# Kernel optimization log

Hardware: AMD Instinct MI355X
Metric: run time of the kernel (lower is better)

Reference implementation:

```python
import jax
import jax.numpy as jnp
from jax import lax
import numpy as np

EMBED_DIM = 768
NUM_HEADS = 12
BATCH = 8
SEQ = 1024
EPS = 1e-07
QK_QBIT = 8
QK_KBIT = 8
AV_ABIT = 8
AV_VBIT = 8
PROJ_WBIT = 8
PROJ_XBIT = 8
SCALE = EMBED_DIM ** (-0.5)  # module uses embed_dim, not head_dim


def _ste(hard, soft):
    # straight-through estimator: forward = hard, backward grad = d(soft)
    return soft + lax.stop_gradient(hard - soft)


def fake_quant_signed(x, bit):
    # _quantize_signed_matrix_train: sign/abs, global-max scaling, STE clamp + round
    sign = lax.stop_gradient(jnp.sign(x))
    a = jnp.abs(x)
    scaling = lax.stop_gradient(jnp.max(a)) + EPS
    y = a / scaling
    y = _ste(jnp.clip(y, 0.0, 1.0), y)          # Clamp.apply (STE)
    levels = 2.0 ** (bit - 1.0) - 1.0
    y = _ste(jnp.round(y * levels) / levels, y)  # Round.apply (STE)
    return y * scaling * sign


def fake_quant_unsigned(x, bit):
    # _quantize_unsigned_matrix_train
    scaling = lax.stop_gradient(jnp.max(x)) + EPS
    y = x / scaling
    y = _ste(jnp.clip(y, 0.0, 1.0), y)
    levels = 2.0 ** bit - 1.0
    y = _ste(jnp.round(y * levels) / levels, y)
    return y * scaling


def asim_linear(x, w, b, wbit, xbit):
    # ASiMLinear in 'Train' mode with signed_act=True: fake-quantize activation
    # and weight, dense matmul, trim_noise=0 -> no perturbation.
    xq = fake_quant_signed(x, xbit)
    wq = fake_quant_signed(w, wbit)
    return jnp.einsum('bnc,oc->bno', xq, wq) + b


def setup_inputs() -> dict:
    key = jax.random.key(0)
    k_x, k_qw, k_qb, k_pw, k_pb = jax.random.split(key, 5)
    x = jax.random.normal(k_x, (BATCH, SEQ, EMBED_DIM), dtype=jnp.float32)
    s = 1.0 / np.sqrt(EMBED_DIM)
    qkv_w = jax.random.normal(k_qw, (3 * EMBED_DIM, EMBED_DIM), dtype=jnp.float32) * s
    qkv_b = jax.random.normal(k_qb, (3 * EMBED_DIM,), dtype=jnp.float32) * 0.01
    proj_w = jax.random.normal(k_pw, (EMBED_DIM, EMBED_DIM), dtype=jnp.float32) * s
    proj_b = jax.random.normal(k_pb, (EMBED_DIM,), dtype=jnp.float32) * 0.01
    return {'x': x, 'qkv_w': qkv_w, 'qkv_b': qkv_b, 'proj_w': proj_w, 'proj_b': proj_b}


def reference(x, qkv_w, qkv_b, proj_w, proj_b):
    B, N, C = x.shape
    H = NUM_HEADS
    D = C // H
    # qkv projection (ASiMLinear, Train mode)
    qkv = asim_linear(x, qkv_w, qkv_b, PROJ_WBIT, PROJ_XBIT)      # [B, N, 3C]
    qkv = qkv.reshape(B, N, 3, H, D).transpose(2, 0, 3, 1, 4)      # [3, B, H, N, D]
    q, k, v = qkv[0], qkv[1], qkv[2]
    # _qk_train: fake-quantize q and k^T, matmul (trim_noise=0 -> no perturb)
    qq = fake_quant_signed(q, QK_QBIT)
    kq = fake_quant_signed(jnp.swapaxes(k, -2, -1), QK_KBIT)
    attn = jnp.einsum('bhnd,bhdm->bhnm', qq, kq) * SCALE           # [B, H, N, N]
    attn = jax.nn.softmax(attn, axis=-1)
    # dropout ratio 0.0 -> identity
    # _av_train: unsigned fake-quant of attention, signed fake-quant of v
    aq = fake_quant_unsigned(attn, AV_ABIT)
    vq = fake_quant_signed(v, AV_VBIT)
    out = jnp.einsum('bhnm,bhmd->bhnd', aq, vq)                    # [B, H, N, D]
    out = out.transpose(0, 2, 1, 3).reshape(B, N, C)
    # output projection (ASiMLinear, Train mode)
    out = asim_linear(out, proj_w, proj_b, PROJ_WBIT, PROJ_XBIT)
    return out
```

## Files before the change

kernel.cpp:

```cpp
#include <hip/hip_runtime.h>
#include <hip/hip_bf16.h>
#include <cstdint>
#include <cstddef>

#define B_    8
#define SEQ_  1024
#define C_    768
#define H_    12
#define D_    64
#define TC_   2304
#define M_    8192
#define EPS_  1e-7f
#define SCALE_ 0.036084391824351615f

typedef __attribute__((ext_vector_type(8))) short bf16x8;
typedef __attribute__((ext_vector_type(4))) float f32x4;

__device__ __forceinline__ bf16x8 expand8(int2 raw) {
  union { int2 v; signed char c[8]; } u; u.v = raw;
  bf16x8 r;
  #pragma unroll
  for (int j = 0; j < 8; ++j) {
    float f = (float)(int)u.c[j];
    r[j] = (short)(__float_as_uint(f) >> 16);
  }
  return r;
}
__device__ __forceinline__ void expand16(int4 raw, int4& lo, int4& hi) {
  union { int4 v; signed char c[16]; } u; u.v = raw;
  unsigned short s[16];
  #pragma unroll
  for (int j = 0; j < 16; ++j) {
    float f = (float)(int)u.c[j];
    s[j] = (unsigned short)(__float_as_uint(f) >> 16);
  }
  lo = *(const int4*)&s[0]; hi = *(const int4*)&s[8];
}

__global__ void k_init(float* g) {
  if (threadIdx.x == 0) {
    g[0]=0.f; g[1]=0.f; g[2]=0.f; g[3]=0.f; g[4]=0.f; g[5]=0.f;
    g[6]=3.402823466e+38f;
    g[7]=0.f;
  }
}

__global__ __launch_bounds__(256) void k_absmax_fused(const float4* __restrict__ x,
                                                      const float4* __restrict__ w1,
                                                      const float4* __restrict__ w2,
                                                      float* g) {
  __shared__ float red[4];
  const int blk = blockIdx.x;
  const float4* p; unsigned n4; float* gout; int b0, nb;
  if (blk < 384)      { p = x;  n4 = 1572864u; gout = &g[0]; b0 = 0;   nb = 384; }
  else if (blk < 480) { p = w1; n4 = 442368u;  gout = &g[1]; b0 = 384; nb = 96;  }
  else                { p = w2; n4 = 147456u;  gout = &g[2]; b0 = 480; nb = 48;  }
  float m = 0.f;
  for (unsigned i = (unsigned)(blk - b0) * 256u + threadIdx.x; i < n4; i += (unsigned)nb * 256u) {
    float4 v = p[i];
    m = fmaxf(m, fmaxf(fmaxf(fabsf(v.x), fabsf(v.y)), fmaxf(fabsf(v.z), fabsf(v.w))));
  }
  #pragma unroll
  for (int off = 32; off; off >>= 1) m = fmaxf(m, __shfl_xor(m, off));
  if ((threadIdx.x & 63) == 0) red[threadIdx.x >> 6] = m;
  __syncthreads();
  if (threadIdx.x == 0) {
    m = fmaxf(fmaxf(red[0], red[1]), fmaxf(red[2], red[3]));
    atomicMax((unsigned int*)gout, __float_as_uint(m));
  }
}

__device__ __forceinline__ void quant_seg8(const float* __restrict__ in, unsigned n, float s,
                                           int8_t* __restrict__ out, unsigned i0, unsigned stride) {
  for (unsigned i = i0; i < n; i += stride) {
    float v = in[i];
    float y = fminf(fabsf(v) / s, 1.0f);
    int q = (int)rintf(y * 127.0f);
    if (v < 0.f) q = -q;
    out[i] = (int8_t)q;
  }
}
__global__ __launch_bounds__(256) void k_quant_fused(const float* __restrict__ x,
                                                     const float* __restrict__ w1,
                                                     const float* __restrict__ w2,
                                                     const float* __restrict__ g,
                                                     int8_t* __restrict__ xq,
                                                     int8_t* __restrict__ wq,
                                                     int8_t* __restrict__ pw) {
  const int blk = blockIdx.x;
  if (blk < 1536)      quant_seg8(x,  6291456u, g[0] + EPS_, xq, (unsigned)blk * 256u + threadIdx.x, 1536u * 256u);
  else if (blk < 1968) quant_seg8(w1, 1769472u, g[1] + EPS_, wq, (unsigned)(blk - 1536) * 256u + threadIdx.x, 432u * 256u);
  else                 quant_seg8(w2,  589824u, g[2] + EPS_, pw, (unsigned)(blk - 1968) * 256u + threadIdx.x, 144u * 256u);
}

__global__ __launch_bounds__(256) void k_quant_i8(const float* __restrict__ in, unsigned n,
                                                  const float* __restrict__ gmax,
                                                  int8_t* __restrict__ out) {
  const float s = *gmax + EPS_;
  quant_seg8(in, n, s, out, blockIdx.x * blockDim.x + threadIdx.x, gridDim.x * blockDim.x);
}

__global__ __launch_bounds__(256) void k_gemm8(const int8_t* __restrict__ A,
                                               const int8_t* __restrict__ Bt,
                                               const float* __restrict__ bias,
                                               float* __restrict__ C,
                                               int Mn, int Nn, int Kn,
                                               const float* __restrict__ sA, const float* __restrict__ sB,
                                               float* pmax, int partDiv) {
  __shared__ unsigned short As[128 * 64];
  __shared__ unsigned short Bs[128 * 64];
  const int tid = threadIdx.x;
  int flat = blockIdx.y * gridDim.x + blockIdx.x;
  int chunk = (gridDim.x * gridDim.y) >> 3;
  int nf = (flat & 7) * chunk + (flat >> 3);
  const int n0 = (nf % gridDim.x) * 128, m0 = (nf / gridDim.x) * 128;
  const int wid = tid >> 6, lane = tid & 63;
  const int wr = wid >> 1, wc = wid & 1;
  const int lrow = lane & 15;
  const int lko = (lane >> 4) << 3;
  f32x4 acc[4][4] = {};
  const int r0 = tid >> 2;
  const int c0 = tid & 3;
  const int8_t* ga = A  + (size_t)m0 * Kn;
  const int8_t* gb = Bt + (size_t)n0 * Kn;
  const int nt = Kn >> 6;
  int4 ra0 = *(const int4*)(ga + (size_t)r0 * Kn + c0 * 16);
  int4 ra1 = *(const int4*)(ga + (size_t)(64 + r0) * Kn + c0 * 16);
  int4 rb0 = *(const int4*)(gb + (size_t)r0 * Kn + c0 * 16);
  int4 rb1 = *(const int4*)(gb + (size_t)(64 + r0) * Kn + c0 * 16);
  for (int t = 0; t < nt; ++t) {
    if (t) __syncthreads();
    {
      int4 lo, hi;
      const int sx0 = (r0 & 7) << 4;
      const int bb0 = r0 * 128 + c0 * 32;
      const int bb1 = (64 + r0) * 128 + c0 * 32;
      expand16(ra0, lo, hi);
      *(int4*)((char*)As + ( bb0       ^ sx0)) = lo;
      *(int4*)((char*)As + ((bb0 + 16) ^ sx0)) = hi;
      expand16(ra1, lo, hi);
      *(int4*)((char*)As + ( bb1       ^ sx0)) = lo;
      *(int4*)((char*)As + ((bb1 + 16) ^ sx0)) = hi;
      expand16(rb0, lo, hi);
      *(int4*)((char*)Bs + ( bb0       ^ sx0)) = lo;
      *(int4*)((char*)Bs + ((bb0 + 16) ^ sx0)) = hi;
      expand16(rb1, lo, hi);
      *(int4*)((char*)Bs + ( bb1       ^ sx0)) = lo;
      *(int4*)((char*)Bs + ((bb1 + 16) ^ sx0)) = hi;
    }
    if (t + 1 < nt) {
      const int ko = (t + 1) * 64;
      ra0 = *(const int4*)(ga + (size_t)r0 * Kn + ko + c0 * 16);
      ra1 = *(const int4*)(ga + (size_t)(64 + r0) * Kn + ko + c0 * 16);
      rb0 = *(const int4*)(gb + (size_t)r0 * Kn + ko + c0 * 16);
      rb1 = *(const int4*)(gb + (size_t)(64 + r0) * Kn + ko + c0 * 16);
    }
    __syncthreads();
    #pragma unroll
    for (int kk = 0; kk < 64; kk += 32) {
      bf16x8 af[4], bfr[4];
      #pragma unroll
      for (int i = 0; i < 4; ++i) {
        int row = wr * 64 + i * 16 + lrow;
        af[i] = *(const bf16x8*)((const char*)As + ((row * 128 + (kk + lko) * 2) ^ ((row & 7) << 4)));
      }
      #pragma unroll
      for (int j = 0; j < 4; ++j) {
        int row = wc * 64 + j * 16 + lrow;
        bfr[j] = *(const bf16x8*)((const char*)Bs + ((row * 128 + (kk + lko) * 2) ^ ((row & 7) << 4)));
      }
      #pragma unroll
      for (int i = 0; i < 4; ++i)
        #pragma unroll
        for (int j = 0; j < 4; ++j)
          acc[i][j] = __builtin_amdgcn_mfma_f32_16x16x32_bf16(af[i], bfr[j], acc[i][j], 0, 0, 0);
    }
  }
  const float alpha = (sA[0] + EPS_) * (sB[0] + EPS_) * (1.0f / 16129.0f);
  const int orow = (lane >> 4) << 2;
  float amax = 0.f;
  #pragma unroll
  for (int i = 0; i < 4; ++i) {
    #pragma unroll
    for (int j = 0; j < 4; ++j) {
      int col = n0 + wc * 64 + j * 16 + lrow;
      float bc = bias[col];
      #pragma unroll
      for (int rr = 0; rr < 4; ++rr) {
        int row = m0 + wr * 64 + i * 16 + orow + rr;
        float val = acc[i][j][rr] * alpha + bc;
        C[(size_t)row * Nn + col] = val;
        amax = fmaxf(amax, fabsf(val));
      }
    }
  }
  if (pmax) {
    #pragma unroll
    for (int off = 32; off; off >>= 1) amax = fmaxf(amax, __shfl_xor(amax, off));
    if (lane == 0) atomicMax((unsigned int*)&pmax[n0 / partDiv], __float_as_uint(amax));
  }
}

__global__ __launch_bounds__(256) void k_quant_heads(const float* __restrict__ qkvf, const float* __restrict__ g,
                                                     int8_t* __restrict__ qo, int8_t* __restrict__ ko,
                                                     int8_t* __restrict__ vT) {
  const unsigned total = (unsigned)M_ * TC_;
  const float s0 = g[3] + EPS_, s1 = g[4] + EPS_, s2 = g[5] + EPS_;
  for (unsigned i = blockIdx.x * blockDim.x + threadIdx.x; i < total; i += gridDim.x * blockDim.x) {
    unsigned m = i / 2304u, o = i % 2304u;
    unsigned part = o / 768u, c = o % 768u;
    unsigned h = c >> 6, d = c & 63;
    unsigned b = m >> 10, n = m & 1023;
    float s = (part == 0) ? s0 : (part == 1) ? s1 : s2;
    float v = qkvf[i];
    float y = fminf(fabsf(v) / s, 1.0f);
    int q = (int)rintf(y * 127.0f);
    if (v < 0.f) q = -q;
    unsigned bh = b * 12 + h;
    if (part == 0)      qo[((size_t)bh * 1024 + n) * 64 + d] = (int8_t)q;
    else if (part == 1) ko[((size_t)bh * 1024 + n) * 64 + d] = (int8_t)q;
    else                vT[((size_t)bh * 64 + d) * 1024 + n] = (int8_t)q;
  }
}

__global__ __launch_bounds__(256) void k_attn_stats_mfma(
    const int8_t* __restrict__ qi8, const int8_t* __restrict__ ki8,
    const float* __restrict__ g, float* __restrict__ rowmax, float* __restrict__ denomv,
    unsigned int* __restrict__ gminden) {
  __shared__ unsigned short Ks[64 * 64];
  __shared__ float red[4];
  const int bh = blockIdx.x >> 4, rt = blockIdx.x & 15;
  const int tid = threadIdx.x, w = tid >> 6, lane = tid & 63;
  const int lrow = lane & 15, lko = (lane >> 4) << 3;
  const int8_t* qbase = qi8 + (size_t)bh * 65536;
  const int8_t* kbase = ki8 + (size_t)bh * 65536;
  bf16x8 qf[2];
  #pragma unroll
  for (int ks = 0; ks < 2; ++ks)
    qf[ks] = expand8(*(const int2*)(qbase + (size_t)(rt*64 + w*16 + lrow) * 64 + ks*32 + lko));
  const float qkScale = (g[3] + EPS_) * (g[4] + EPS_) * (1.0f / 16129.0f) * SCALE_;
  float m = -3.0e38f, den = 0.f;
  const int srow = tid >> 2, sc = tid & 3;
  const int sx = (srow & 7) << 4;
  int4 kraw = *(const int4*)(kbase + (size_t)srow * 64 + sc * 16);
  for (int t = 0; t < 16; ++t) {
    __syncthreads();
    {
      int4 lo, hi; expand16(kraw, lo, hi);
      int bb = srow * 128 + sc * 32;
      *(int4*)((char*)Ks + ( bb       ^ sx)) = lo;
      *(int4*)((char*)Ks + ((bb + 16) ^ sx)) = hi;
    }
    if (t < 15)
      kraw = *(const int4*)(kbase + (size_t)(t + 1) * 4096 + (size_t)srow * 64 + sc * 16);
    __syncthreads();
    f32x4 acc[4] = {};
    #pragma unroll
    for (int ks = 0; ks < 2; ++ks)
      #pragma unroll
      for (int j = 0; j < 4; ++j) {
        int row = j * 16 + lrow;
        bf16x8 kf = *(const bf16x8*)((const char*)Ks + ((row * 128 + (ks*32 + lko) * 2) ^ ((row & 7) << 4)));
        acc[j] = __builtin_amdgcn_mfma_f32_16x16x32_bf16(kf, qf[ks], acc[j], 0, 0, 0);
      }
    float mnew = m;
    #pragma unroll
    for (int j = 0; j < 4; ++j)
      #pragma unroll
      for (int rr = 0; rr < 4; ++rr)
        mnew = fmaxf(mnew, acc[j][rr] * qkScale);
    float d = den * __expf(m - mnew);
    #pragma unroll
    for (int j = 0; j < 4; ++j)
      #pragma unroll
      for (int rr = 0; rr < 4; ++rr)
        d += __expf(acc[j][rr] * qkScale - mnew);
    den = d; m = mnew;
  }
  #pragma unroll
  for (int off = 16; off <= 32; off <<= 1) {
    float mo = __shfl_xor(m, off);
    float doo = __shfl_xor(den, off);
    float mg = fmaxf(m, mo);
    den = den * __expf(m - mg) + doo * __expf(mo - mg);
    m = mg;
  }
  if (lane < 16) {
    size_t rg = (size_t)bh * 1024 + rt * 64 + w * 16 + lane;
    rowmax[rg] = m;
    denomv[rg] = den;
  }
  float bm = den;
  #pragma unroll
  for (int off = 1; off < 16; off <<= 1) bm = fminf(bm, __shfl_xor(bm, off));
  if (lane == 0) red[w] = bm;
  __syncthreads();
  if (tid == 0)
    atomicMin(gminden, __float_as_uint(fminf(fminf(red[0], red[1]), fminf(red[2], red[3]))));
}

__global__ __launch_bounds__(256) void k_attn_pv_mfma(
    const int8_t* __restrict__ qi8, const int8_t* __restrict__ ki8, const int8_t* __restrict__ vti8,
    const float* __restrict__ g, const unsigned int* __restrict__ gminden,
    const float* __restrict__ rowmax, const float* __restrict__ denomv,
    float* __restrict__ aof, float* __restrict__ gamax) {
  __shared__ unsigned short Ks[64 * 64];
  __shared__ unsigned short Vs[64 * 64];
  __shared__ unsigned short Ps[64 * 64];
  __shared__ float red[4];
  const int bh = blockIdx.x >> 4, rt = blockIdx.x & 15;
  const int b = bh / 12, h = bh % 12;
  const int tid = threadIdx.x, w = tid >> 6, lane = tid & 63;
  const int lrow = lane & 15, lko = (lane >> 4) << 3;
  const int8_t* qbase = qi8 + (size_t)bh * 65536;
  const int8_t* kbase = ki8 + (size_t)bh * 65536;
  const int8_t* vbase = vti8 + (size_t)bh * 65536;
  bf16x8 qf[2];
  #pragma unroll
  for (int ks = 0; ks < 2; ++ks)
    qf[ks] = expand8(*(const int2*)(qbase + (size_t)(rt*64 + w*16 + lrow) * 64 + ks*32 + lko));
  const float qkScale = (g[3] + EPS_) * (g[4] + EPS_) * (1.0f / 16129.0f) * SCALE_;
  const float minden = __uint_as_float(*gminden);
  const float sa = 1.0f / minden + EPS_;
  const float invSa = 1.0f / sa;
  const float sv = g[5] + EPS_;
  const float pvScale = sa * sv * (1.0f / 32385.0f);
  const float rm  = rowmax[(size_t)bh * 1024 + rt * 64 + w * 16 + lrow];
  const float ivd = 1.0f / denomv[(size_t)bh * 1024 + rt * 64 + w * 16 + lrow];
  f32x4 accO[4] = {};
  const int srow = tid >> 2, sc = tid & 3;
  const int sx = (srow & 7) << 4;
  int4 kraw = *(const int4*)(kbase + (size_t)srow * 64 + sc * 16);
  int4 vraw = *(const int4*)(vbase + (size_t)srow * 1024 + sc * 16);
  for (int t = 0; t < 16; ++t) {
    __syncthreads();
    {
      int4 lo, hi;
      int bb = srow * 128 + sc * 32;
      expand16(kraw, lo, hi);
      *(int4*)((char*)Ks + ( bb       ^ sx)) = lo;
      *(int4*)((char*)Ks + ((bb + 16) ^ sx)) = hi;
      expand16(vraw, lo, hi);
      *(int4*)((char*)Vs + ( bb       ^ sx)) = lo;
      *(int4*)((char*)Vs + ((bb + 16) ^ sx)) = hi;
    }
    if (t < 15) {
      kraw = *(const int4*)(kbase + (size_t)(t + 1) * 4096 + (size_t)srow * 64 + sc * 16);
      vraw = *(const int4*)(vbase + (size_t)srow * 1024 + (t + 1) * 64 + sc * 16);
    }
    __syncthreads();
    f32x4 acc[4] = {};
    #pragma unroll
    for (int ks = 0; ks < 2; ++ks)
      #pragma unroll
      for (int j = 0; j < 4; ++j) {
        int row = j * 16 + lrow;
        bf16x8 kf = *(const bf16x8*)((const char*)Ks + ((row * 128 + (ks*32 + lko) * 2) ^ ((row & 7) << 4)));
        acc[j] = __builtin_amdgcn_mfma_f32_16x16x32_bf16(kf, qf[ks], acc[j], 0, 0, 0);
      }
    const int q = w * 16 + lrow;
    const int kb = (lane >> 4) << 2;
    #pragma unroll
    for (int j = 0; j < 4; ++j) {
      float a0 = rintf(fminf(__expf(acc[j][0] * qkScale - rm) * ivd * invSa, 1.0f) * 255.0f);
      float a1 = rintf(fminf(__expf(acc[j][1] * qkScale - rm) * ivd * invSa, 1.0f) * 255.0f);
      float a2 = rintf(fminf(__expf(acc[j][2] * qkScale - rm) * ivd * invSa, 1.0f) * 255.0f);
      float a3 = rintf(fminf(__expf(acc[j][3] * qkScale - rm) * ivd * invSa, 1.0f) * 255.0f);
      uint2 pk;
      pk.x = (__float_as_uint(a0) >> 16) | ((__float_as_uint(a1) >> 16) << 16);
      pk.y = (__float_as_uint(a2) >> 16) | ((__float_as_uint(a3) >> 16) << 16);
      int byteoff = (q * 128 + (j * 16 + kb) * 2) ^ ((q & 7) << 4);
      *(uint2*)((char*)Ps + byteoff) = pk;
    }
    #pragma unroll
    for (int ks = 0; ks < 2; ++ks) {
      bf16x8 pf = *(const bf16x8*)((const char*)Ps + ((q * 128 + (ks*32 + lko) * 2) ^ ((q & 7) << 4)));
      #pragma unroll
      for (int j = 0; j < 4; ++j) {
        int row = j * 16 + lrow;
        bf16x8 vf = *(const bf16x8*)((const char*)Vs + ((row * 128 + (ks*32 + lko) * 2) ^ ((row & 7) << 4)));
        accO[j] = __builtin_amdgcn_mfma_f32_16x16x32_bf16(pf, vf, accO[j], 0, 0, 0);
      }
    }
  }
  float amax = 0.f;
  #pragma unroll
  for (int j = 0; j < 4; ++j) {
    int d = j * 16 + lrow;
    #pragma unroll
    for (int rr = 0; rr < 4; ++rr) {
      int row = rt * 64 + w * 16 + (lane >> 4) * 4 + rr;
      float val = accO[j][rr] * pvScale;
      aof[((size_t)(b * 1024 + row)) * 768 + h * 64 + d] = val;
      amax = fmaxf(amax, fabsf(val));
    }
  }
  #pragma unroll
  for (int off = 1; off < 64; off <<= 1) amax = fmaxf(amax, __shfl_xor(amax, off));
  if (lane == 0) red[w] = amax;
  __syncthreads();
  if (tid == 0)
    atomicMax((unsigned int*)gamax, __float_as_uint(fmaxf(fmaxf(red[0], red[1]), fmaxf(red[2], red[3]))));
}

extern "C" void kernel_launch(void* const* d_in, const int* in_sizes, int n_in,
                              void* d_out, int out_size, void* d_ws, size_t ws_size,
                              hipStream_t stream) {
  const float* x      = (const float*)d_in[0];
  const float* qkv_w  = (const float*)d_in[1];
  const float* qkv_b  = (const float*)d_in[2];
  const float* proj_w = (const float*)d_in[3];
  const float* proj_b = (const float*)d_in[4];
  float* out = (float*)d_out;

  char* w = (char*)d_ws;
  float*          g      = (float*)(w + 0);
  float*          rowmax = (float*)(w + 256);
  float*          denomv = (float*)(w + 393472);
  int8_t*         qi8    = (int8_t*)(w + 786688);
  int8_t*         ki8    = (int8_t*)(w + 7078144);
  int8_t*         vT     = (int8_t*)(w + 13369600);
  int8_t*         pw8    = (int8_t*)(w + 19661056);
  int8_t*         xq8    = (int8_t*)(w + 20840704);
  int8_t*         wq8    = (int8_t*)(w + 33423616);
  float*          qkvf   = (float*)(w + 36962560);
  float*          aof    = (float*)(w + 36962560);
  int8_t*         aob8   = (int8_t*)(w + 62128384);

  hipLaunchKernelGGL(k_init, dim3(1), dim3(64), 0, stream, g);

  hipLaunchKernelGGL(k_absmax_fused, dim3(528), dim3(256), 0, stream,
                     (const float4*)x, (const float4*)qkv_w, (const float4*)proj_w, g);

  hipLaunchKernelGGL(k_quant_fused, dim3(2112), dim3(256), 0, stream,
                     x, qkv_w, proj_w, g, xq8, wq8, pw8);

  hipLaunchKernelGGL(k_gemm8, dim3(TC_ / 128, M_ / 128), dim3(256), 0, stream,
                     xq8, wq8, qkv_b, qkvf, M_, TC_, C_, &g[0], &g[1], &g[3], 768);

  hipLaunchKernelGGL(k_quant_heads, dim3(2048), dim3(256), 0, stream, qkvf, g, qi8, ki8, vT);

  hipLaunchKernelGGL(k_attn_stats_mfma, dim3(1536), dim3(256), 0, stream,
                     qi8, ki8, g, rowmax, denomv, (unsigned int*)&g[6]);
  hipLaunchKernelGGL(k_attn_pv_mfma, dim3(1536), dim3(256), 0, stream,
                     qi8, ki8, vT, g, (const unsigned int*)&g[6], rowmax, denomv, aof, &g[7]);

  hipLaunchKernelGGL(k_quant_i8, dim3(2048), dim3(256), 0, stream, aof, 6291456u, &g[7], aob8);

  hipLaunchKernelGGL(k_gemm8, dim3(C_ / 128, M_ / 128), dim3(256), 0, stream,
                     aob8, pw8, proj_b, out, M_, C_, C_, &g[7], &g[2], (float*)nullptr, 1);

  (void)in_sizes; (void)n_in; (void)out_size; (void)ws_size;
}
```

Measured before the change: 269.4 us.

## Use native int8 MFMA in GEMMs and tile the head quantization kernel

The projection GEMMs now feed the int8 operands straight into the i32 16x16x64 i8 MFMA, replacing the path that expanded int8 to bf16 in shared memory and ran the bf16 MFMA. This removes the conversion ALU work and halves the LDS footprint. Separately, the per-head quantization kernel now gives each block one 64-row tile of one (batch, head), writes q/k with 16-byte stores, and transposes v through shared memory so the vT writes are coalesced. Integer accumulation is exact for these 8-bit inputs, but the new LDS layout with no swizzle may cause bank conflicts.

Measured after the change: 236.4 us. 1.14x faster.

```diff
diff --git a/kernel.cpp b/kernel.cpp
--- a/kernel.cpp
+++ b/kernel.cpp
@@ -15,6 +15,7 @@
 
 typedef __attribute__((ext_vector_type(8))) short bf16x8;
 typedef __attribute__((ext_vector_type(4))) float f32x4;
+typedef __attribute__((ext_vector_type(4))) int   i32x4;
 
 __device__ __forceinline__ bf16x8 expand8(int2 raw) {
   union { int2 v; signed char c[8]; } u; u.v = raw;
@@ -35,6 +36,12 @@
     s[j] = (unsigned short)(__float_as_uint(f) >> 16);
   }
   lo = *(const int4*)&s[0]; hi = *(const int4*)&s[8];
+}
+
+__device__ __forceinline__ int8_t quant1(float v, float s) {
+  float y = fminf(fabsf(v) / s, 1.0f);
+  int q = (int)rintf(y * 127.0f);
+  return (int8_t)(v < 0.f ? -q : q);
 }
 
 __global__ void k_init(float* g) {
@@ -72,13 +79,8 @@
 
 __device__ __forceinline__ void quant_seg8(const float* __restrict__ in, unsigned n, float s,
                                            int8_t* __restrict__ out, unsigned i0, unsigned stride) {
-  for (unsigned i = i0; i < n; i += stride) {
-    float v = in[i];
-    float y = fminf(fabsf(v) / s, 1.0f);
-    int q = (int)rintf(y * 127.0f);
-    if (v < 0.f) q = -q;
-    out[i] = (int8_t)q;
-  }
+  for (unsigned i = i0; i < n; i += stride)
+    out[i] = quant1(in[i], s);
 }
 __global__ __launch_bounds__(256) void k_quant_fused(const float* __restrict__ x,
                                                      const float* __restrict__ w1,
@@ -100,15 +102,15 @@
   quant_seg8(in, n, s, out, blockIdx.x * blockDim.x + threadIdx.x, gridDim.x * blockDim.x);
 }
 
-__global__ __launch_bounds__(256) void k_gemm8(const int8_t* __restrict__ A,
-                                               const int8_t* __restrict__ Bt,
-                                               const float* __restrict__ bias,
-                                               float* __restrict__ C,
-                                               int Mn, int Nn, int Kn,
-                                               const float* __restrict__ sA, const float* __restrict__ sB,
-                                               float* pmax, int partDiv) {
-  __shared__ unsigned short As[128 * 64];
-  __shared__ unsigned short Bs[128 * 64];
+__global__ __launch_bounds__(256) void k_gemm8i(const int8_t* __restrict__ A,
+                                                const int8_t* __restrict__ Bt,
+                                                const float* __restrict__ bias,
+                                                float* __restrict__ C,
+                                                int Mn, int Nn, int Kn,
+                                                const float* __restrict__ sA, const float* __restrict__ sB,
+                                                float* pmax, int partDiv) {
+  __shared__ int8_t As[4][128][16];
+  __shared__ int8_t Bs[4][128][16];
   const int tid = threadIdx.x;
   int flat = blockIdx.y * gridDim.x + blockIdx.x;
   int chunk = (gridDim.x * gridDim.y) >> 3;
@@ -117,64 +119,41 @@
   const int wid = tid >> 6, lane = tid & 63;
   const int wr = wid >> 1, wc = wid & 1;
   const int lrow = lane & 15;
-  const int lko = (lane >> 4) << 3;
-  f32x4 acc[4][4] = {};
-  const int r0 = tid >> 2;
-  const int c0 = tid & 3;
-  const int8_t* ga = A  + (size_t)m0 * Kn;
-  const int8_t* gb = Bt + (size_t)n0 * Kn;
+  const int lslot = lane >> 4;
+  i32x4 acc[4][4] = {};
+  const int srow = tid & 127;
+  const int slot0 = tid >> 7;
+  const int8_t* ga = A  + (size_t)(m0 + srow) * Kn + slot0 * 16;
+  const int8_t* gb = Bt + (size_t)(n0 + srow) * Kn + slot0 * 16;
   const int nt = Kn >> 6;
-  int4 ra0 = *(const int4*)(ga + (size_t)r0 * Kn + c0 * 16);
-  int4 ra1 = *(const int4*)(ga + (size_t)(64 + r0) * Kn + c0 * 16);
-  int4 rb0 = *(const int4*)(gb + (size_t)r0 * Kn + c0 * 16);
-  int4 rb1 = *(const int4*)(gb + (size_t)(64 + r0) * Kn + c0 * 16);
+  int4 ra0 = *(const int4*)(ga);
+  int4 ra1 = *(const int4*)(ga + 32);
+  int4 rb0 = *(const int4*)(gb);
+  int4 rb1 = *(const int4*)(gb + 32);
   for (int t = 0; t < nt; ++t) {
     if (t) __syncthreads();
-    {
-      int4 lo, hi;
-      const int sx0 = (r0 & 7) << 4;
-      const int bb0 = r0 * 128 + c0 * 32;
-      const int bb1 = (64 + r0) * 128 + c0 * 32;
-      expand16(ra0, lo, hi);
-      *(int4*)((char*)As + ( bb0       ^ sx0)) = lo;
-      *(int4*)((char*)As + ((bb0 + 16) ^ sx0)) = hi;
-      expand16(ra1, lo, hi);
-      *(int4*)((char*)As + ( bb1       ^ sx0)) = lo;
-      *(int4*)((char*)As + ((bb1 + 16) ^ sx0)) = hi;
-      expand16(rb0, lo, hi);
-      *(int4*)((char*)Bs + ( bb0       ^ sx0)) = lo;
-      *(int4*)((char*)Bs + ((bb0 + 16) ^ sx0)) = hi;
-      expand16(rb1, lo, hi);
-      *(int4*)((char*)Bs + ( bb1       ^ sx0)) = lo;
-      *(int4*)((char*)Bs + ((bb1 + 16) ^ sx0)) = hi;
-    }
+    *(int4*)&As[slot0][srow][0]     = ra0;
+    *(int4*)&As[slot0 + 2][srow][0] = ra1;
+    *(int4*)&Bs[slot0][srow][0]     = rb0;
+    *(int4*)&Bs[slot0 + 2][srow][0] = rb1;
     if (t + 1 < nt) {
       const int ko = (t + 1) * 64;
-      ra0 = *(const int4*)(ga + (size_t)r0 * Kn + ko + c0 * 16);
-      ra1 = *(const int4*)(ga + (size_t)(64 + r0) * Kn + ko + c0 * 16);
-      rb0 = *(const int4*)(gb + (size_t)r0 * Kn + ko + c0 * 16);
-      rb1 = *(const int4*)(gb + (size_t)(64 + r0) * Kn + ko + c0 * 16);
+      ra0 = *(const int4*)(ga + ko);
+      ra1 = *(const int4*)(ga + ko + 32);
+      rb0 = *(const int4*)(gb + ko);
+      rb1 = *(const int4*)(gb + ko + 32);
     }
     __syncthreads();
-    #pragma unroll
-    for (int kk = 0; kk < 64; kk += 32) {
-      bf16x8 af[4], bfr[4];
-      #pragma unroll
-      for (int i = 0; i < 4; ++i) {
-        int row = wr * 64 + i * 16 + lrow;
-        af[i] = *(const bf16x8*)((const char*)As + ((row * 128 + (kk + lko) * 2) ^ ((row & 7) << 4)));
-      }
-      #pragma unroll
-      for (int j = 0; j < 4; ++j) {
-        int row = wc * 64 + j * 16 + lrow;
-        bfr[j] = *(const bf16x8*)((const char*)Bs + ((row * 128 + (kk + lko) * 2) ^ ((row & 7) << 4)));
-      }
-      #pragma unroll
-      for (int i = 0; i < 4; ++i)
-        #pragma unroll
-        for (int j = 0; j < 4; ++j)
-          acc[i][j] = __builtin_amdgcn_mfma_f32_16x16x32_bf16(af[i], bfr[j], acc[i][j], 0, 0, 0);
-    }
+    i32x4 af[4], bfr[4];
+    #pragma unroll
+    for (int i = 0; i < 4; ++i) af[i]  = *(const i32x4*)&As[lslot][wr * 64 + i * 16 + lrow][0];
+    #pragma unroll
+    for (int j = 0; j < 4; ++j) bfr[j] = *(const i32x4*)&Bs[lslot][wc * 64 + j * 16 + lrow][0];
+    #pragma unroll
+    for (int i = 0; i < 4; ++i)
+      #pragma unroll
+      for (int j = 0; j < 4; ++j)
+        acc[i][j] = __builtin_amdgcn_mfma_i32_16x16x64_i8(af[i], bfr[j], acc[i][j], 0, 0, 0);
   }
   const float alpha = (sA[0] + EPS_) * (sB[0] + EPS_) * (1.0f / 16129.0f);
   const int orow = (lane >> 4) << 2;
@@ -188,7 +167,7 @@
       #pragma unroll
       for (int rr = 0; rr < 4; ++rr) {
         int row = m0 + wr * 64 + i * 16 + orow + rr;
-        float val = acc[i][j][rr] * alpha + bc;
+        float val = (float)acc[i][j][rr] * alpha + bc;
         C[(size_t)row * Nn + col] = val;
         amax = fmaxf(amax, fabsf(val));
       }
@@ -204,22 +183,38 @@
 __global__ __launch_bounds__(256) void k_quant_heads(const float* __restrict__ qkvf, const float* __restrict__ g,
                                                      int8_t* __restrict__ qo, int8_t* __restrict__ ko,
                                                      int8_t* __restrict__ vT) {
-  const unsigned total = (unsigned)M_ * TC_;
+  __shared__ float vt[64][65];
+  const int bh = blockIdx.x >> 4, nt = blockIdx.x & 15;
+  const int b = bh / 12, h = bh % 12;
+  const int n0 = nt * 64;
+  const int tid = threadIdx.x;
   const float s0 = g[3] + EPS_, s1 = g[4] + EPS_, s2 = g[5] + EPS_;
-  for (unsigned i = blockIdx.x * blockDim.x + threadIdx.x; i < total; i += gridDim.x * blockDim.x) {
-    unsigned m = i / 2304u, o = i % 2304u;
-    unsigned part = o / 768u, c = o % 768u;
-    unsigned h = c >> 6, d = c & 63;
-    unsigned b = m >> 10, n = m & 1023;
-    float s = (part == 0) ? s0 : (part == 1) ? s1 : s2;
-    float v = qkvf[i];
-    float y = fminf(fabsf(v) / s, 1.0f);
-    int q = (int)rintf(y * 127.0f);
-    if (v < 0.f) q = -q;
-    unsigned bh = b * 12 + h;
-    if (part == 0)      qo[((size_t)bh * 1024 + n) * 64 + d] = (int8_t)q;
-    else if (part == 1) ko[((size_t)bh * 1024 + n) * 64 + d] = (int8_t)q;
-    else                vT[((size_t)bh * 64 + d) * 1024 + n] = (int8_t)q;
+  const int r = tid >> 2, dc = tid & 3;
+  const size_t mrow = (size_t)(b * 1024 + n0 + r) * 2304;
+  union { int4 v; int8_t c[16]; } pk;
+  {
+    const float* src = qkvf + mrow + h * 64 + dc * 16;
+    #pragma unroll
+    for (int e = 0; e < 16; ++e) pk.c[e] = quant1(src[e], s0);
+    *(int4*)&qo[((size_t)bh * 1024 + n0 + r) * 64 + dc * 16] = pk.v;
+  }
+  {
+    const float* src = qkvf + mrow + 768 + h * 64 + dc * 16;
+    #pragma unroll
+    for (int e = 0; e < 16; ++e) pk.c[e] = quant1(src[e], s1);
+    *(int4*)&ko[((size_t)bh * 1024 + n0 + r) * 64 + dc * 16] = pk.v;
+  }
+  {
+    const float* src = qkvf + mrow + 1536 + h * 64 + dc * 16;
+    #pragma unroll
+    for (int e = 0; e < 16; ++e) vt[dc * 16 + e][r] = src[e];
+  }
+  __syncthreads();
+  {
+    const int d = tid >> 2, nc = tid & 3;
+    #pragma unroll
+    for (int e = 0; e < 16; ++e) pk.c[e] = quant1(vt[d][nc * 16 + e], s2);
+    *(int4*)&vT[((size_t)bh * 64 + d) * 1024 + n0 + nc * 16] = pk.v;
   }
 }
 
@@ -435,10 +430,10 @@
   hipLaunchKernelGGL(k_quant_fused, dim3(2112), dim3(256), 0, stream,
                      x, qkv_w, proj_w, g, xq8, wq8, pw8);
 
-  hipLaunchKernelGGL(k_gemm8, dim3(TC_ / 128, M_ / 128), dim3(256), 0, stream,
+  hipLaunchKernelGGL(k_gemm8i, dim3(TC_ / 128, M_ / 128), dim3(256), 0, stream,
                      xq8, wq8, qkv_b, qkvf, M_, TC_, C_, &g[0], &g[1], &g[3], 768);
 
-  hipLaunchKernelGGL(k_quant_heads, dim3(2048), dim3(256), 0, stream, qkvf, g, qi8, ki8, vT);
+  hipLaunchKernelGGL(k_quant_heads, dim3(1536), dim3(256), 0, stream, qkvf, g, qi8, ki8, vT);
 
   hipLaunchKernelGGL(k_attn_stats_mfma, dim3(1536), dim3(256), 0, stream,
                      qi8, ki8, g, rowmax, denomv, (unsigned int*)&g[6]);
@@ -447,7 +442,7 @@
 
   hipLaunchKernelGGL(k_quant_i8, dim3(2048), dim3(256), 0, stream, aof, 6291456u, &g[7], aob8);
 
-  hipLaunchKernelGGL(k_gemm8, dim3(C_ / 128, M_ / 128), dim3(256), 0, stream,
+  hipLaunchKernelGGL(k_gemm8i, dim3(C_ / 128, M_ / 128), dim3(256), 0, stream,
                      aob8, pw8, proj_b, out, M_, C_, C_, &g[7], &g[2], (float*)nullptr, 1);
 
   (void)in_sizes; (void)n_in; (void)out_size; (void)ws_size;
```
